# Performance work log

Hardware: AMD Instinct MI355X
Metric: run time of the kernel (lower is better)

Reference implementation:

```python
import jax, jax.numpy as jnp
import numpy as np

N_QUBITS = 12
DIM = 2 ** N_QUBITS
BATCH = 2048


def setup_inputs() -> dict:
    key = jax.random.key(0)
    k1, k2, k3 = jax.random.split(key, 3)
    inputs = jax.random.normal(k1, (BATCH, N_QUBITS), dtype=jnp.float32)
    weight = jax.random.normal(k2, (3 + 2 * N_QUBITS,), dtype=jnp.float32)
    entangle_matrix = jax.random.normal(k3, (DIM, DIM), dtype=jnp.float32)
    return {"inputs": inputs, "weight": weight, "entangle_matrix": entangle_matrix}


def _encode(ry_angles, rz_angles):
    # Encoder: state = prod over qubits of first column of (Rz*Ry) per qubit.
    ry = ry_angles / 2
    rz = rz_angles / 2
    a = jnp.cos(ry) * jnp.exp(-1j * rz)  # entry11 (row bit = 0)
    b = jnp.sin(ry) * jnp.exp(1j * rz)   # entry21 (row bit = 1)
    col2 = jnp.stack([a, b], axis=-1).astype(jnp.complex64)  # [B, n, 2]
    B, n = ry.shape
    v = jnp.ones((B, 1), dtype=jnp.complex64)
    for q in range(n):  # Kronecker fold over qubits (big-endian, matches dec2bin)
        v = (v[:, :, None] * col2[:, q][:, None, :]).reshape(B, -1)
    return v  # [B, 2^n]


def _rot_mat(w):
    # rot_mat: per-qubit Rx(w[q]) @ Rz(w[n+q]), then full Kronecker product.
    n = w.shape[0] // 2
    tx = (w[:n] / 2).astype(jnp.complex64)
    tz = (w[n:] / 2).astype(jnp.complex64)
    c, s = jnp.cos(tx), jnp.sin(tx)
    rx = jnp.stack([jnp.stack([c, -1j * s], -1),
                    jnp.stack([-1j * s, c], -1)], -2)  # [n,2,2]
    ez = jnp.exp(-1j * tz)
    zero = jnp.zeros_like(ez)
    rz = jnp.stack([jnp.stack([ez, zero], -1),
                    jnp.stack([zero, jnp.exp(1j * tz)], -1)], -2)  # [n,2,2]
    mats = jnp.einsum('qij,qjk->qik', rx, rz)
    M = mats[0]
    for q in range(1, n):
        M = jnp.kron(M, mats[q])
    return M  # [2^n, 2^n]


def _ry2(theta):
    a = theta / 2
    c, s = jnp.cos(a), jnp.sin(a)
    return jnp.stack([jnp.stack([c, -s]), jnp.stack([s, c])])  # [2,2] real


def _final_rot(th3):
    # final_rot_mat: Rz-form @ Ry-form @ Rx-form (all ry_mat_list), kron with identity.
    rot = _ry2(th3[2]) @ (_ry2(th3[1]) @ _ry2(th3[0]))
    eye = jnp.eye(DIM // 2, dtype=jnp.complex64)
    return jnp.kron(rot.astype(jnp.complex64), eye)  # [DIM, DIM]


def reference(inputs, weight, entangle_matrix):
    # initial=False branch
    ry_angles = inputs
    rz_angles = jnp.square(inputs)
    v = _encode(ry_angles, rz_angles)                 # [B, DIM] complex64
    E = entangle_matrix.astype(jnp.complex64)
    R = _rot_mat(weight[3:])
    M = E @ R @ E                                     # [DIM, DIM]
    v = v @ M.T                                       # tensordot dims ([-1],[-1])
    F = _final_rot(weight[:3])
    v = v @ F.T
    half = DIM // 2
    # vector[:, half:] = 0 then sum |.|^2  <=>  sum over first half
    return jnp.sum(jnp.square(jnp.abs(v[:, :half])), axis=-1)  # [B] float32
```

## Files before the change

### kernel.cpp

```cpp
#include <hip/hip_runtime.h>
#include <math.h>

#define QDIM 4096
#define NQ 12
#define QBATCH 2048

typedef _Float16 f16x8 __attribute__((ext_vector_type(8)));
typedef float f32x4 __attribute__((ext_vector_type(4)));
typedef int i32x4 __attribute__((ext_vector_type(4)));

__device__ __forceinline__ void gld_lds16(const void* gptr, void* ldsptr) {
    __builtin_amdgcn_global_load_lds(
        (const __attribute__((address_space(1))) void*)gptr,
        (__attribute__((address_space(3))) void*)ldsptr,
        16, 0, 0);
}

__device__ __forceinline__ int q8(float x) {
    float y = fminf(fmaxf(x, -127.f), 127.f);
    return (int)rintf(y);
}
__device__ __forceinline__ int pack4_i8(int a, int b, int c, int d) {
    return (a & 0xFF) | ((b & 0xFF) << 8) | ((c & 0xFF) << 16) | ((d & 0xFF) << 24);
}

__global__ __launch_bounds__(256) void conv_kernel(
    const float* __restrict__ E, const float* __restrict__ wgt,
    _Float16* __restrict__ Eh, signed char* __restrict__ G8)
{
    float th = 0.5f * (wgt[0] + wgt[1] + wgt[2]);
    float c0 = cosf(th), c1 = -sinf(th);
    const float qs = 127.f / 6.f;
    size_t flat = ((size_t)blockIdx.x * 256 + threadIdx.x) * 8;
    size_t n = flat >> 12;
    size_t k = flat & (QDIM - 1);
    const float* p0 = E + n * QDIM + k;
    const float* p1 = p0 + (size_t)QBATCH * QDIM;
    float4 a0 = ((const float4*)p0)[0], a1 = ((const float4*)p0)[1];
    float4 b0 = ((const float4*)p1)[0], b1 = ((const float4*)p1)[1];
    f16x8 h0 = { (_Float16)a0.x, (_Float16)a0.y, (_Float16)a0.z, (_Float16)a0.w,
                 (_Float16)a1.x, (_Float16)a1.y, (_Float16)a1.z, (_Float16)a1.w };
    f16x8 h1 = { (_Float16)b0.x, (_Float16)b0.y, (_Float16)b0.z, (_Float16)b0.w,
                 (_Float16)b1.x, (_Float16)b1.y, (_Float16)b1.z, (_Float16)b1.w };
    *(f16x8*)&Eh[n * QDIM + k] = h0;
    *(f16x8*)&Eh[(n + QBATCH) * QDIM + k] = h1;
    float g[8] = { c0*a0.x + c1*b0.x, c0*a0.y + c1*b0.y, c0*a0.z + c1*b0.z, c0*a0.w + c1*b0.w,
                   c0*a1.x + c1*b1.x, c0*a1.y + c1*b1.y, c0*a1.z + c1*b1.z, c0*a1.w + c1*b1.w };
    int2 gp = { pack4_i8(q8(g[0]*qs), q8(g[1]*qs), q8(g[2]*qs), q8(g[3]*qs)),
                pack4_i8(q8(g[4]*qs), q8(g[5]*qs), q8(g[6]*qs), q8(g[7]*qs)) };
    *(int2*)&G8[n * QDIM + k] = gp;
}

__global__ __launch_bounds__(256) void expand_kernel(
    const float* __restrict__ inputs, _Float16* __restrict__ A1,
    float* __restrict__ out)
{
    __shared__ float ab[NQ][4];
    const int b = blockIdx.x;
    const int tid = threadIdx.x;
    if (tid == 0) out[b] = 0.f;
    if (tid < NQ) {
        float x = inputs[b * NQ + tid];
        float ry = 0.5f * x;
        float rz = 0.5f * x * x;
        float ca = cosf(ry), sa = sinf(ry), cz = cosf(rz), sz = sinf(rz);
        ab[tid][0] = ca * cz;  ab[tid][1] = -ca * sz;
        ab[tid][2] = sa * cz;  ab[tid][3] =  sa * sz;
    }
    __syncthreads();
    float pr0 = 1.f, pi0 = 0.f;
#pragma unroll
    for (int q = 0; q < 8; ++q) {
        int bit = (tid >> (7 - q)) & 1;
        float cr = ab[q][bit * 2 + 0], ci = ab[q][bit * 2 + 1];
        float nr = pr0 * cr - pi0 * ci;
        float ni = pr0 * ci + pi0 * cr;
        pr0 = nr; pi0 = ni;
    }
    f16x8 vr[2], vi[2];
#pragma unroll
    for (int u = 0; u < 16; ++u) {
        float pr = pr0, pi = pi0;
#pragma unroll
        for (int q = 8; q < 12; ++q) {
            int bit = (u >> (11 - q)) & 1;
            float cr = ab[q][bit * 2 + 0], ci = ab[q][bit * 2 + 1];
            float nr = pr * cr - pi * ci;
            float ni = pr * ci + pi * cr;
            pr = nr; pi = ni;
        }
        vr[u >> 3][u & 7] = (_Float16)pr;
        vi[u >> 3][u & 7] = (_Float16)pi;
    }
    const int idx0 = tid * 16;
    *(f16x8*)&A1[(size_t)b * QDIM + idx0] = vr[0];
    *(f16x8*)&A1[(size_t)b * QDIM + idx0 + 8] = vr[1];
    *(f16x8*)&A1[(size_t)(b + QBATCH) * QDIM + idx0] = vi[0];
    *(f16x8*)&A1[(size_t)(b + QBATCH) * QDIM + idx0 + 8] = vi[1];
}

#define VMCNT(N_) asm volatile("s_waitcnt vmcnt(" #N_ ")" ::: "memory")
#define LGKM0()   asm volatile("s_waitcnt lgkmcnt(0)" ::: "memory")
#define LGKM8()   asm volatile("s_waitcnt lgkmcnt(8)" ::: "memory")
#define SBAR()                              \
    do {                                    \
        asm volatile("" ::: "memory");      \
        __builtin_amdgcn_s_barrier();       \
        asm volatile("" ::: "memory");      \
    } while (0)

__global__ __launch_bounds__(512, 2) void gemm_f16_256(
    const _Float16* __restrict__ A, const _Float16* __restrict__ B,
    _Float16* __restrict__ C, int N)
{
    const int K = QDIM;
    __shared__ __attribute__((aligned(16))) _Float16 As[2][256 * 64];
    __shared__ __attribute__((aligned(16))) _Float16 Bs[2][256 * 64];

    const int tid  = threadIdx.x;
    const int wave = tid >> 6;
    const int lane = tid & 63;
    const int bm0 = blockIdx.y * 256;
    const int bn0 = blockIdx.x * 256;
    const int wm0 = (wave >> 2) * 128;
    const int wn0 = (wave & 3) * 64;
    const int q = lane >> 4;
    const int r = lane & 15;
    const int rx = r & 7;

    f32x4 acc[8][4];
#pragma unroll
    for (int i = 0; i < 8; ++i)
#pragma unroll
        for (int j = 0; j < 4; ++j) acc[i][j] = (f32x4){0.f, 0.f, 0.f, 0.f};

    const int srow = tid >> 3;
    const int scol = ((tid & 7) ^ (srow & 7)) * 8;
    const _Float16* gA = A + (size_t)(bm0 + srow) * K + scol;
    const _Float16* gB = B + (size_t)(bn0 + srow) * K + scol;

#define STG_A(D, KK, NN) gld_lds16(gA + (size_t)(NN) * 64 * K + (KK), &As[D][(NN) * 4096 + wave * 512])
#define STG_B(D, KK, NN) gld_lds16(gB + (size_t)(NN) * 64 * K + (KK), &Bs[D][(NN) * 4096 + wave * 512])
#define STG_AH(D, KK, H) do { STG_A(D, KK, 2*(H)); STG_A(D, KK, 2*(H)+1); } while (0)
#define STG_BH(D, KK, H) do { STG_B(D, KK, 2*(H)); STG_B(D, KK, 2*(H)+1); } while (0)

#define RD_A4(DST, D, IB)                                                          \
    _Pragma("unroll")                                                              \
    for (int ii = 0; ii < 4; ++ii) {                                               \
        _Pragma("unroll")                                                          \
        for (int ss = 0; ss < 2; ++ss)                                             \
            DST[ii][ss] = *(const f16x8*)&As[D][(wm0 + ((IB) + ii) * 16 + r) * 64  \
                                                + (((ss * 4 + q) ^ rx) * 8)];      \
    }
#define RD_B2(DST, D, JB)                                                          \
    _Pragma("unroll")                                                              \
    for (int jj = 0; jj < 2; ++jj) {                                               \
        _Pragma("unroll")                                                          \
        for (int ss = 0; ss < 2; ++ss)                                             \
            DST[jj][ss] = *(const f16x8*)&Bs[D][(wn0 + ((JB) + jj) * 16 + r) * 64  \
                                                + (((ss * 4 + q) ^ rx) * 8)];      \
    }
#define MM8(AR, BR, I0, J0)                                                        \
    _Pragma("unroll")                                                              \
    for (int ii = 0; ii < 4; ++ii) {                                               \
        _Pragma("unroll")                                                          \
        for (int jj = 0; jj < 2; ++jj) {                                           \
            acc[(I0) + ii][(J0) + jj] = __builtin_amdgcn_mfma_f32_16x16x32_f16(    \
                AR[ii][0], BR[jj][0], acc[(I0) + ii][(J0) + jj], 0, 0, 0);         \
            acc[(I0) + ii][(J0) + jj] = __builtin_amdgcn_mfma_f32_16x16x32_f16(    \
                AR[ii][1], BR[jj][1], acc[(I0) + ii][(J0) + jj], 0, 0, 0);         \
        }                                                                          \
    }

    f16x8 a0[4][2], a1[4][2], b0[2][2], b1[2][2];

    STG_AH(0, 0, 0); STG_AH(0, 0, 1);
    STG_BH(0, 0, 0); STG_BH(0, 0, 1);
    STG_BH(1, 64, 0); STG_BH(1, 64, 1);
    VMCNT(4);
    SBAR();

    for (int tau = 0; tau < 32; ++tau) {
        const int k1 = (2 * tau + 1) * 64;
        const int k2 = ((2 * tau + 2) & 63) * 64;
        const int k3 = ((2 * tau + 3) & 63) * 64;

        RD_A4(a0, 0, 0); RD_B2(b0, 0, 0); RD_B2(b1, 0, 2);
        STG_AH(1, k1, 0); STG_AH(1, k1, 1);
        LGKM8();
        SBAR(); LGKM0();
        __builtin_amdgcn_s_setprio(1);
        MM8(a0, b0, 0, 0);
        MM8(a0, b1, 0, 2);
        __builtin_amdgcn_s_setprio(0);
        SBAR();

        RD_A4(a1, 0, 4);
        STG_BH(0, k2, 0); STG_BH(0, k2, 1);
        VMCNT(4);
        SBAR(); LGKM0();
        __builtin_amdgcn_s_setprio(1);
        MM8(a1, b1, 4, 2);
        MM8(a1, b0, 4, 0);
        __builtin_amdgcn_s_setprio(0);
        SBAR();

        RD_A4(a0, 1, 0); RD_B2(b0, 1, 0); RD_B2(b1, 1, 2);
        STG_AH(0, k2, 0); STG_AH(0, k2, 1);
        LGKM8();
        SBAR(); LGKM0();
        __builtin_amdgcn_s_setprio(1);
        MM8(a0, b0, 0, 0);
        MM8(a0, b1, 0, 2);
        __builtin_amdgcn_s_setprio(0);
        SBAR();

        RD_A4(a1, 1, 4);
        STG_BH(1, k3, 0); STG_BH(1, k3, 1);
        VMCNT(4);
        SBAR(); LGKM0();
        __builtin_amdgcn_s_setprio(1);
        MM8(a1, b1, 4, 2);
        MM8(a1, b0, 4, 0);
        __builtin_amdgcn_s_setprio(0);
        SBAR();
    }
    VMCNT(0);

#pragma unroll
    for (int i = 0; i < 8; ++i) {
        const int crow = bm0 + wm0 + i * 16 + q * 4;
#pragma unroll
        for (int rr = 0; rr < 4; ++rr)
#pragma unroll
            for (int j = 0; j < 4; ++j)
                C[(size_t)(crow + rr) * N + bn0 + wn0 + j * 16 + r] = (_Float16)acc[i][j][rr];
    }
#undef STG_A
#undef STG_B
#undef STG_AH
#undef STG_BH
#undef RD_A4
#undef RD_B2
#undef MM8
}

__global__ __launch_bounds__(256) void butterfly_kernel(
    const _Float16* __restrict__ u1, const float* __restrict__ wgt,
    signed char* __restrict__ A2, float* __restrict__ scaleA)
{
    __shared__ float sRe[4366];
    __shared__ float sIm[4366];
    __shared__ float mats[NQ][8];
    __shared__ float red[8];
    const int blk = blockIdx.x;
    const int tid = threadIdx.x;
    const int ah = tid >> 4;
    const int al = tid & 15;

    if (tid < NQ) {
        float tx = 0.5f * wgt[3 + tid];
        float tz = 0.5f * wgt[15 + tid];
        float c = cosf(tx), s = sinf(tx), cz = cosf(tz), sz = sinf(tz);
        mats[tid][0] =  c * cz;  mats[tid][1] = -c * sz;
        mats[tid][2] =  s * sz;  mats[tid][3] = -s * cz;
        mats[tid][4] = -s * sz;  mats[tid][5] = -s * cz;
        mats[tid][6] =  c * cz;  mats[tid][7] =  c * sz;
    }

    float xr[16], xi[16];
    {
        const _Float16* pRe = u1 + (size_t)blk * QDIM + tid * 16;
        const _Float16* pIm = u1 + (size_t)(blk + QBATCH) * QDIM + tid * 16;
        f16x8 r0 = ((const f16x8*)pRe)[0], r1 = ((const f16x8*)pRe)[1];
        f16x8 i0 = ((const f16x8*)pIm)[0], i1 = ((const f16x8*)pIm)[1];
#pragma unroll
        for (int j = 0; j < 8; ++j) {
            xr[j] = (float)r0[j]; xr[8 + j] = (float)r1[j];
            xi[j] = (float)i0[j]; xi[8 + j] = (float)i1[j];
        }
    }
    __syncthreads();

#define BFLY_STAGE(arrR, arrI, K_, Q_)                                         \
    {                                                                          \
        const float m00r = mats[Q_][0], m00i = mats[Q_][1];                    \
        const float m01r = mats[Q_][2], m01i = mats[Q_][3];                    \
        const float m10r = mats[Q_][4], m10i = mats[Q_][5];                    \
        const float m11r = mats[Q_][6], m11i = mats[Q_][7];                    \
        _Pragma("unroll")                                                      \
        for (int t = 0; t < 8; ++t) {                                          \
            int i0 = ((t >> (K_)) << ((K_) + 1)) | (t & ((1 << (K_)) - 1));    \
            int i1 = i0 | (1 << (K_));                                         \
            float x0r = arrR[i0], x0i = arrI[i0];                              \
            float x1r = arrR[i1], x1i = arrI[i1];                              \
            arrR[i0] = m00r * x0r - m00i * x0i + m01r * x1r - m01i * x1i;      \
            arrI[i0] = m00r * x0i + m00i * x0r + m01r * x1i + m01i * x1r;      \
            arrR[i1] = m10r * x0r - m10i * x0i + m11r * x1r - m11i * x1i;      \
            arrI[i1] = m10r * x0i + m10i * x0r + m11r * x1i + m11i * x1r;      \
        }                                                                      \
    }

#pragma unroll
    for (int p = 0; p < 4; ++p) BFLY_STAGE(xr, xi, p, 11 - p);

#pragma unroll
    for (int c = 0; c < 16; ++c) {
        sRe[273 * ah + 17 * al + c] = xr[c];
        sIm[273 * ah + 17 * al + c] = xi[c];
    }
    __syncthreads();

    float yr[16], yi[16];
#pragma unroll
    for (int b = 0; b < 16; ++b) {
        yr[b] = sRe[273 * ah + 17 * b + al];
        yi[b] = sIm[273 * ah + 17 * b + al];
    }
#pragma unroll
    for (int p = 0; p < 4; ++p) BFLY_STAGE(yr, yi, p, 7 - p);

#pragma unroll
    for (int b = 0; b < 16; ++b) {
        sRe[273 * ah + 17 * b + al] = yr[b];
        sIm[273 * ah + 17 * b + al] = yi[b];
    }
    __syncthreads();

    float zr[16], zi[16];
#pragma unroll
    for (int a = 0; a < 16; ++a) {
        zr[a] = sRe[273 * a + 17 * ah + al];
        zi[a] = sIm[273 * a + 17 * ah + al];
    }
#pragma unroll
    for (int p = 0; p < 4; ++p) BFLY_STAGE(zr, zi, p, 3 - p);

    float mR = 0.f, mI = 0.f;
#pragma unroll
    for (int j = 0; j < 16; ++j) {
        mR = fmaxf(mR, fabsf(zr[j]));
        mI = fmaxf(mI, fabsf(zi[j]));
    }
#pragma unroll
    for (int off = 32; off > 0; off >>= 1) {
        mR = fmaxf(mR, __shfl_xor(mR, off, 64));
        mI = fmaxf(mI, __shfl_xor(mI, off, 64));
    }
    const int wid = tid >> 6;
    if ((tid & 63) == 0) { red[wid] = mR; red[4 + wid] = mI; }
    __syncthreads();
    mR = fmaxf(fmaxf(red[0], red[1]), fmaxf(red[2], red[3]));
    mI = fmaxf(fmaxf(red[4], red[5]), fmaxf(red[6], red[7]));
    mR = fmaxf(mR, 1e-30f);
    mI = fmaxf(mI, 1e-30f);
    if (tid == 0) {
        scaleA[blk] = mR / 127.f;
        scaleA[blk + QBATCH] = mI / 127.f;
    }
    const float invR = 127.f / mR, invI = 127.f / mI;

    signed char* oRe = A2 + (size_t)blk * QDIM + ah * 16 + al;
    signed char* oIm = A2 + (size_t)(blk + QBATCH) * QDIM + ah * 16 + al;
#pragma unroll
    for (int a = 0; a < 16; ++a) {
        oRe[a * 256] = (signed char)q8(zr[a] * invR);
        oIm[a * 256] = (signed char)q8(zi[a] * invI);
    }
#undef BFLY_STAGE
}

__global__ __launch_bounds__(512, 2) void gemm2_i8_256(
    const signed char* __restrict__ A, const signed char* __restrict__ B,
    const float* __restrict__ scaleA, float* __restrict__ out)
{
    const int K = QDIM;
    __shared__ __attribute__((aligned(16))) signed char As[2][256 * 128];
    __shared__ __attribute__((aligned(16))) signed char Bs[2][128 * 128];

    const int tid  = threadIdx.x;
    const int wave = tid >> 6;
    const int lane = tid & 63;
    const int bn0 = blockIdx.x * 128;
    const int bm0 = blockIdx.y * 256;
    const int wm0 = (wave >> 1) * 64;
    const int wn0 = (wave & 1) * 64;
    const int q = lane >> 4;
    const int r = lane & 15;
    const int rx = r & 7;

    i32x4 acc[4][4];
#pragma unroll
    for (int i = 0; i < 4; ++i)
#pragma unroll
        for (int j = 0; j < 4; ++j) acc[i][j] = (i32x4){0, 0, 0, 0};

    const int srow = tid >> 3;
    const int scol = ((tid & 7) ^ (srow & 7)) * 16;
    const signed char* gA = A + (size_t)(bm0 + srow) * K + scol;
    const signed char* gB = B + (size_t)(bn0 + srow) * K + scol;

#define STG2_A(D, KK, NN) gld_lds16(gA + (size_t)(NN) * 64 * K + (KK), &As[D][(NN) * 8192 + wave * 1024])
#define STG2_B(D, KK, NN) gld_lds16(gB + (size_t)(NN) * 64 * K + (KK), &Bs[D][(NN) * 8192 + wave * 1024])

#define RD2_A(DST, D, IB)                                                           \
    _Pragma("unroll")                                                               \
    for (int ii = 0; ii < 2; ++ii) {                                                \
        _Pragma("unroll")                                                           \
        for (int ss = 0; ss < 2; ++ss)                                              \
            DST[ii][ss] = *(const i32x4*)&As[D][(wm0 + ((IB) + ii) * 16 + r) * 128  \
                                                + (((ss * 4 + q) ^ rx) * 16)];      \
    }
#define RD2_B(DST, D, JB)                                                           \
    _Pragma("unroll")                                                               \
    for (int jj = 0; jj < 2; ++jj) {                                                \
        _Pragma("unroll")                                                           \
        for (int ss = 0; ss < 2; ++ss)                                              \
            DST[jj][ss] = *(const i32x4*)&Bs[D][(wn0 + ((JB) + jj) * 16 + r) * 128  \
                                                + (((ss * 4 + q) ^ rx) * 16)];      \
    }
#define MM2(AR, BR, I0, J0)                                                         \
    _Pragma("unroll")                                                               \
    for (int ii = 0; ii < 2; ++ii) {                                                \
        _Pragma("unroll")                                                           \
        for (int jj = 0; jj < 2; ++jj) {                                            \
            acc[(I0) + ii][(J0) + jj] = __builtin_amdgcn_mfma_i32_16x16x64_i8(      \
                AR[ii][0], BR[jj][0], acc[(I0) + ii][(J0) + jj], 0, 0, 0);          \
            acc[(I0) + ii][(J0) + jj] = __builtin_amdgcn_mfma_i32_16x16x64_i8(      \
                AR[ii][1], BR[jj][1], acc[(I0) + ii][(J0) + jj], 0, 0, 0);          \
        }                                                                           \
    }

    i32x4 a0[2][2], a1[2][2], b0[2][2], b1[2][2];

    STG2_B(0, 0, 0); STG2_B(0, 0, 1);
    STG2_A(0, 0, 0); STG2_A(0, 0, 1); STG2_A(0, 0, 2); STG2_A(0, 0, 3);
    STG2_B(1, 128, 0); STG2_B(1, 128, 1);
    VMCNT(2);
    SBAR();

    for (int tau = 0; tau < 16; ++tau) {
        const int k1 = (2 * tau + 1) * 128;
        const int k2 = ((2 * tau + 2) & 31) * 128;
        const int k3 = ((2 * tau + 3) & 31) * 128;

        RD2_A(a0, 0, 0); RD2_B(b0, 0, 0);
        STG2_A(1, k1, 0); STG2_A(1, k1, 1);
        SBAR(); LGKM0();
        __builtin_amdgcn_s_setprio(1);
        MM2(a0, b0, 0, 0);
        __builtin_amdgcn_s_setprio(0);
        SBAR();

        RD2_B(b1, 0, 2);
        STG2_A(1, k1, 2); STG2_A(1, k1, 3);
        SBAR(); LGKM0();
        __builtin_amdgcn_s_setprio(1);
        MM2(a0, b1, 0, 2);
        __builtin_amdgcn_s_setprio(0);
        SBAR();

        RD2_A(a1, 0, 2);
        SBAR(); LGKM0();
        __builtin_amdgcn_s_setprio(1);
        MM2(a1, b1, 2, 2);
        __builtin_amdgcn_s_setprio(0);
        SBAR();

        STG2_B(0, k2, 0); STG2_B(0, k2, 1);
        VMCNT(2);
        SBAR(); LGKM0();
        __builtin_amdgcn_s_setprio(1);
        MM2(a1, b0, 2, 0);
        __builtin_amdgcn_s_setprio(0);
        SBAR();

        RD2_A(a0, 1, 0); RD2_B(b0, 1, 0);
        STG2_A(0, k2, 0); STG2_A(0, k2, 1);
        SBAR(); LGKM0();
        __builtin_amdgcn_s_setprio(1);
        MM2(a0, b0, 0, 0);
        __builtin_amdgcn_s_setprio(0);
        SBAR();

        RD2_B(b1, 1, 2);
        STG2_A(0, k2, 2); STG2_A(0, k2, 3);
        SBAR(); LGKM0();
        __builtin_amdgcn_s_setprio(1);
        MM2(a0, b1, 0, 2);
        __builtin_amdgcn_s_setprio(0);
        SBAR();

        RD2_A(a1, 1, 2);
        SBAR(); LGKM0();
        __builtin_amdgcn_s_setprio(1);
        MM2(a1, b1, 2, 2);
        __builtin_amdgcn_s_setprio(0);
        SBAR();

        STG2_B(1, k3, 0); STG2_B(1, k3, 1);
        VMCNT(2);
        SBAR(); LGKM0();
        __builtin_amdgcn_s_setprio(1);
        MM2(a1, b0, 2, 0);
        __builtin_amdgcn_s_setprio(0);
        SBAR();
    }
    VMCNT(0);

    const float dqG = 6.f / 127.f;
#pragma unroll
    for (int i = 0; i < 4; ++i) {
#pragma unroll
        for (int rr = 0; rr < 4; ++rr) {
            const int row = bm0 + wm0 + i * 16 + q * 4 + rr;
            const float sc = scaleA[row] * dqG;
            float v = 0.f;
#pragma unroll
            for (int j = 0; j < 4; ++j) {
                float t = sc * (float)acc[i][j][rr];
                v = fmaf(t, t, v);
            }
            v += __shfl_xor(v, 1, 64);
            v += __shfl_xor(v, 2, 64);
            v += __shfl_xor(v, 4, 64);
            v += __shfl_xor(v, 8, 64);
            if (r == 0) atomicAdd(&out[row & (QBATCH - 1)], v);
        }
    }
#undef STG2_A
#undef STG2_B
#undef RD2_A
#undef RD2_B
#undef MM2
}

extern "C" void kernel_launch(void* const* d_in, const int* in_sizes, int n_in,
                              void* d_out, int out_size, void* d_ws, size_t ws_size,
                              hipStream_t stream)
{
    const float* inputs = (const float*)d_in[0];
    const float* weight = (const float*)d_in[1];
    const float* E      = (const float*)d_in[2];
    float* out = (float*)d_out;

    char* ws = (char*)d_ws;
    const size_t MB = 1024 * 1024;
    _Float16*    Eh     = (_Float16*)   (ws + 0);
    signed char* G8     = (signed char*)(ws + 32 * MB);
    _Float16*    A1     = (_Float16*)   (ws + 40 * MB);
    _Float16*    u1     = (_Float16*)   (ws + 72 * MB);
    signed char* A2     = (signed char*)(ws + 104 * MB);
    float*       scaleA = (float*)      (ws + 120 * MB);

    conv_kernel<<<(QBATCH * QDIM / 8) / 256, 256, 0, stream>>>(E, weight, Eh, G8);
    expand_kernel<<<QBATCH, 256, 0, stream>>>(inputs, A1, out);
    gemm_f16_256<<<dim3(QDIM / 256, QDIM / 256), 512, 0, stream>>>(A1, Eh, u1, QDIM);
    butterfly_kernel<<<QBATCH, 256, 0, stream>>>(u1, weight, A2, scaleA);
    gemm2_i8_256<<<dim3(2048 / 128, QDIM / 256), 512, 0, stream>>>(A2, G8, scaleA, out);
}
```

Before: 300.8 us.

## Shrink first GEMM tile to 256x128 with rotated register-prefetch pipeline

The f16 GEMM block tile narrows from 256x256 to 256x128, with waves laid out 4x2 instead of 2x4 and each wave holding a 64x64 accumulator. This halves accumulator registers and B shared memory and doubles the grid to 512 blocks on the 256-CU part. The main loop becomes a four-phase schedule that prefetches the next A/B fragments into registers while MFMAs run, with sched_barrier fences and reordered waitcnts. The cost is lower arithmetic intensity per block, since A is refetched twice as often, plus more barriers per k-step.

```diff
diff --git a/kernel.cpp b/kernel.cpp
--- a/kernel.cpp
+++ b/kernel.cpp
@@ -101,7 +101,7 @@
 
 #define VMCNT(N_) asm volatile("s_waitcnt vmcnt(" #N_ ")" ::: "memory")
 #define LGKM0()   asm volatile("s_waitcnt lgkmcnt(0)" ::: "memory")
-#define LGKM8()   asm volatile("s_waitcnt lgkmcnt(8)" ::: "memory")
+#define SCHED0()  __builtin_amdgcn_sched_barrier(0)
 #define SBAR()                              \
     do {                                    \
         asm volatile("" ::: "memory");      \
@@ -115,22 +115,22 @@
 {
     const int K = QDIM;
     __shared__ __attribute__((aligned(16))) _Float16 As[2][256 * 64];
-    __shared__ __attribute__((aligned(16))) _Float16 Bs[2][256 * 64];
+    __shared__ __attribute__((aligned(16))) _Float16 Bs[2][128 * 64];
 
     const int tid  = threadIdx.x;
     const int wave = tid >> 6;
     const int lane = tid & 63;
     const int bm0 = blockIdx.y * 256;
-    const int bn0 = blockIdx.x * 256;
-    const int wm0 = (wave >> 2) * 128;
-    const int wn0 = (wave & 3) * 64;
+    const int bn0 = blockIdx.x * 128;
+    const int wm0 = (wave >> 1) * 64;
+    const int wn0 = (wave & 1) * 64;
     const int q = lane >> 4;
     const int r = lane & 15;
     const int rx = r & 7;
 
-    f32x4 acc[8][4];
-#pragma unroll
-    for (int i = 0; i < 8; ++i)
+    f32x4 acc[4][4];
+#pragma unroll
+    for (int i = 0; i < 4; ++i)
 #pragma unroll
         for (int j = 0; j < 4; ++j) acc[i][j] = (f32x4){0.f, 0.f, 0.f, 0.f};
 
@@ -141,94 +141,90 @@
 
 #define STG_A(D, KK, NN) gld_lds16(gA + (size_t)(NN) * 64 * K + (KK), &As[D][(NN) * 4096 + wave * 512])
 #define STG_B(D, KK, NN) gld_lds16(gB + (size_t)(NN) * 64 * K + (KK), &Bs[D][(NN) * 4096 + wave * 512])
-#define STG_AH(D, KK, H) do { STG_A(D, KK, 2*(H)); STG_A(D, KK, 2*(H)+1); } while (0)
-#define STG_BH(D, KK, H) do { STG_B(D, KK, 2*(H)); STG_B(D, KK, 2*(H)+1); } while (0)
-
-#define RD_A4(DST, D, IB)                                                          \
+#define STG_AT(D, KK) do { STG_A(D, KK, 0); STG_A(D, KK, 1); STG_A(D, KK, 2); STG_A(D, KK, 3); } while (0)
+#define STG_BT(D, KK) do { STG_B(D, KK, 0); STG_B(D, KK, 1); } while (0)
+
+#define RD_A2(DST, D, IB)                                                          \
     _Pragma("unroll")                                                              \
-    for (int ii = 0; ii < 4; ++ii) {                                               \
+    for (int ii = 0; ii < 2; ++ii) {                                               \
         _Pragma("unroll")                                                          \
         for (int ss = 0; ss < 2; ++ss)                                             \
             DST[ii][ss] = *(const f16x8*)&As[D][(wm0 + ((IB) + ii) * 16 + r) * 64  \
                                                 + (((ss * 4 + q) ^ rx) * 8)];      \
     }
-#define RD_B2(DST, D, JB)                                                          \
+#define RD_B4(DST, D)                                                              \
     _Pragma("unroll")                                                              \
-    for (int jj = 0; jj < 2; ++jj) {                                               \
+    for (int jj = 0; jj < 4; ++jj) {                                               \
         _Pragma("unroll")                                                          \
         for (int ss = 0; ss < 2; ++ss)                                             \
-            DST[jj][ss] = *(const f16x8*)&Bs[D][(wn0 + ((JB) + jj) * 16 + r) * 64  \
+            DST[jj][ss] = *(const f16x8*)&Bs[D][(wn0 + jj * 16 + r) * 64           \
                                                 + (((ss * 4 + q) ^ rx) * 8)];      \
     }
-#define MM8(AR, BR, I0, J0)                                                        \
+#define MM16(AR, BR, I0)                                                           \
     _Pragma("unroll")                                                              \
-    for (int ii = 0; ii < 4; ++ii) {                                               \
+    for (int ii = 0; ii < 2; ++ii) {                                               \
         _Pragma("unroll")                                                          \
-        for (int jj = 0; jj < 2; ++jj) {                                           \
-            acc[(I0) + ii][(J0) + jj] = __builtin_amdgcn_mfma_f32_16x16x32_f16(    \
-                AR[ii][0], BR[jj][0], acc[(I0) + ii][(J0) + jj], 0, 0, 0);         \
-            acc[(I0) + ii][(J0) + jj] = __builtin_amdgcn_mfma_f32_16x16x32_f16(    \
-                AR[ii][1], BR[jj][1], acc[(I0) + ii][(J0) + jj], 0, 0, 0);         \
+        for (int jj = 0; jj < 4; ++jj) {                                           \
+            acc[(I0) + ii][jj] = __builtin_amdgcn_mfma_f32_16x16x32_f16(           \
+                AR[ii][0], BR[jj][0], acc[(I0) + ii][jj], 0, 0, 0);                \
+            acc[(I0) + ii][jj] = __builtin_amdgcn_mfma_f32_16x16x32_f16(           \
+                AR[ii][1], BR[jj][1], acc[(I0) + ii][jj], 0, 0, 0);                \
         }                                                                          \
     }
 
-    f16x8 a0[4][2], a1[4][2], b0[2][2], b1[2][2];
-
-    STG_AH(0, 0, 0); STG_AH(0, 0, 1);
-    STG_BH(0, 0, 0); STG_BH(0, 0, 1);
-    STG_BH(1, 64, 0); STG_BH(1, 64, 1);
-    VMCNT(4);
+    f16x8 aLo0[2][2], aHi0[2][2], aLo1[2][2], aHi1[2][2], b0[4][2], b1[4][2];
+
+    STG_BT(0, 0); STG_AT(0, 0);
+    STG_BT(1, 64); STG_AT(1, 64);
+    VMCNT(6);
     SBAR();
+    RD_A2(aLo0, 0, 0);
+    RD_B4(b0, 0);
 
     for (int tau = 0; tau < 32; ++tau) {
-        const int k1 = (2 * tau + 1) * 64;
         const int k2 = ((2 * tau + 2) & 63) * 64;
         const int k3 = ((2 * tau + 3) & 63) * 64;
 
-        RD_A4(a0, 0, 0); RD_B2(b0, 0, 0); RD_B2(b1, 0, 2);
-        STG_AH(1, k1, 0); STG_AH(1, k1, 1);
-        LGKM8();
-        SBAR(); LGKM0();
-        __builtin_amdgcn_s_setprio(1);
-        MM8(a0, b0, 0, 0);
-        MM8(a0, b1, 0, 2);
-        __builtin_amdgcn_s_setprio(0);
-        SBAR();
-
-        RD_A4(a1, 0, 4);
-        STG_BH(0, k2, 0); STG_BH(0, k2, 1);
-        VMCNT(4);
-        SBAR(); LGKM0();
-        __builtin_amdgcn_s_setprio(1);
-        MM8(a1, b1, 4, 2);
-        MM8(a1, b0, 4, 0);
-        __builtin_amdgcn_s_setprio(0);
-        SBAR();
-
-        RD_A4(a0, 1, 0); RD_B2(b0, 1, 0); RD_B2(b1, 1, 2);
-        STG_AH(0, k2, 0); STG_AH(0, k2, 1);
-        LGKM8();
-        SBAR(); LGKM0();
-        __builtin_amdgcn_s_setprio(1);
-        MM8(a0, b0, 0, 0);
-        MM8(a0, b1, 0, 2);
-        __builtin_amdgcn_s_setprio(0);
-        SBAR();
-
-        RD_A4(a1, 1, 4);
-        STG_BH(1, k3, 0); STG_BH(1, k3, 1);
-        VMCNT(4);
-        SBAR(); LGKM0();
-        __builtin_amdgcn_s_setprio(1);
-        MM8(a1, b1, 4, 2);
-        MM8(a1, b0, 4, 0);
-        __builtin_amdgcn_s_setprio(0);
-        SBAR();
+        SBAR(); LGKM0(); SBAR(); SCHED0();
+        STG_BT(0, k2);
+        RD_A2(aHi0, 0, 2);
+        SCHED0();
+        __builtin_amdgcn_s_setprio(1);
+        MM16(aLo0, b0, 0);
+        __builtin_amdgcn_s_setprio(0);
+
+        VMCNT(2);
+        SBAR(); LGKM0(); SBAR(); SCHED0();
+        STG_AT(0, k2);
+        RD_A2(aLo1, 1, 0);
+        RD_B4(b1, 1);
+        SCHED0();
+        __builtin_amdgcn_s_setprio(1);
+        MM16(aHi0, b0, 2);
+        __builtin_amdgcn_s_setprio(0);
+
+        SBAR(); LGKM0(); SBAR(); SCHED0();
+        STG_BT(1, k3);
+        RD_A2(aHi1, 1, 2);
+        SCHED0();
+        __builtin_amdgcn_s_setprio(1);
+        MM16(aLo1, b1, 0);
+        __builtin_amdgcn_s_setprio(0);
+
+        VMCNT(2);
+        SBAR(); LGKM0(); SBAR(); SCHED0();
+        STG_AT(1, k3);
+        RD_A2(aLo0, 0, 0);
+        RD_B4(b0, 0);
+        SCHED0();
+        __builtin_amdgcn_s_setprio(1);
+        MM16(aHi1, b1, 2);
+        __builtin_amdgcn_s_setprio(0);
     }
     VMCNT(0);
 
 #pragma unroll
-    for (int i = 0; i < 8; ++i) {
+    for (int i = 0; i < 4; ++i) {
         const int crow = bm0 + wm0 + i * 16 + q * 4;
 #pragma unroll
         for (int rr = 0; rr < 4; ++rr)
@@ -238,11 +234,11 @@
     }
 #undef STG_A
 #undef STG_B
-#undef STG_AH
-#undef STG_BH
-#undef RD_A4
-#undef RD_B2
-#undef MM8
+#undef STG_AT
+#undef STG_BT
+#undef RD_A2
+#undef RD_B4
+#undef MM16
 }
 
 __global__ __launch_bounds__(256) void butterfly_kernel(
@@ -555,7 +551,7 @@
 
     conv_kernel<<<(QBATCH * QDIM / 8) / 256, 256, 0, stream>>>(E, weight, Eh, G8);
     expand_kernel<<<QBATCH, 256, 0, stream>>>(inputs, A1, out);
-    gemm_f16_256<<<dim3(QDIM / 256, QDIM / 256), 512, 0, stream>>>(A1, Eh, u1, QDIM);
+    gemm_f16_256<<<dim3(QDIM / 128, QDIM / 256), 512, 0, stream>>>(A1, Eh, u1, QDIM);
     butterfly_kernel<<<QBATCH, 256, 0, stream>>>(u1, weight, A2, scaleA);
     gemm2_i8_256<<<dim3(2048 / 128, QDIM / 256), 512, 0, stream>>>(A2, G8, scaleA, out);
 }
```

After: 324.3 us. 7.8% more time.
